# Kernel optimization log

Measured on AMD Instinct MI355X. Metric: run time of the kernel, lower is better.

## Reference

```python
import jax, jax.numpy as jnp
import numpy as np

HID = 512
HEADS = 8
PF = 2048
EPS = 1e-5


def _layernorm(x, g, b):
    mu = jnp.mean(x, axis=-1, keepdims=True)
    var = jnp.var(x, axis=-1, keepdims=True)
    return (x - mu) * jax.lax.rsqrt(var + EPS) * g + b


def setup_inputs() -> dict:
    key = jax.random.key(0)
    ks = jax.random.split(key, 20)
    s = 0.02
    inp = {
        "trg": jax.random.normal(ks[0], (16, 1024, HID), jnp.float32),
        "src": jax.random.normal(ks[1], (16, 1024, HID), jnp.float32),
        "ln_g": jnp.ones((HID,), jnp.float32),
        "ln_b": jnp.zeros((HID,), jnp.float32),
        "wq": jax.random.normal(ks[2], (HID, HID), jnp.float32) * s,
        "bq": jnp.zeros((HID,), jnp.float32),
        "wk": jax.random.normal(ks[3], (HID, HID), jnp.float32) * s,
        "bk": jnp.zeros((HID,), jnp.float32),
        "wv": jax.random.normal(ks[4], (HID, HID), jnp.float32) * s,
        "bv": jnp.zeros((HID,), jnp.float32),
        "wo": jax.random.normal(ks[5], (HID, HID), jnp.float32) * s,
        "bo": jnp.zeros((HID,), jnp.float32),
        "pf1_w": jax.random.normal(ks[6], (PF, HID), jnp.float32) * s,
        "pf1_b": jnp.zeros((PF,), jnp.float32),
        "pf2_w": jax.random.normal(ks[7], (HID, PF), jnp.float32) * s,
        "pf2_b": jnp.zeros((HID,), jnp.float32),
        "fc1_w": jax.random.normal(ks[8], (256, HID), jnp.float32) * s,
        "fc1_b": jnp.zeros((256,), jnp.float32),
        "fc2_w": jax.random.normal(ks[9], (2, 256), jnp.float32) * s,
        "fc2_b": jnp.zeros((2,), jnp.float32),
    }
    return inp


def reference(trg, src, ln_g, ln_b, wq, bq, wk, bk, wv, bv, wo, bo,
              pf1_w, pf1_b, pf2_w, pf2_b, fc1_w, fc1_b, fc2_w, fc2_b):
    B, T, D = trg.shape
    S = src.shape[1]
    dh = D // HEADS

    # --- multi-head attention (Q=trg, K=V=src, no mask; dropout=eval/no-op) ---
    q = (trg @ wq.T + bq).reshape(B, T, HEADS, dh)
    k = (src @ wk.T + bk).reshape(B, S, HEADS, dh)
    v = (src @ wv.T + bv).reshape(B, S, HEADS, dh)
    scores = jnp.einsum('bqhd,bkhd->bhqk', q, k) / jnp.sqrt(jnp.float32(dh))
    attn = jax.nn.softmax(scores, axis=-1)
    ctx = jnp.einsum('bhqk,bkhd->bqhd', attn, v).reshape(B, T, D)
    sa_out = ctx @ wo.T + bo

    x = _layernorm(trg + sa_out, ln_g, ln_b)

    # --- position-wise feed-forward ---
    h = jax.nn.relu(x @ pf1_w.T + pf1_b)
    ff = h @ pf2_w.T + pf2_b
    x = _layernorm(x + ff, ln_g, ln_b)

    # --- norm-weighted sum pooling over sequence (vectorized) ---
    norm = jnp.linalg.norm(x, axis=2)              # [B, T]
    w = jax.nn.softmax(norm, axis=1)               # [B, T]
    pooled = jnp.einsum('bt,btd->bd', w, x)        # [B, D]

    label = jax.nn.relu(pooled @ fc1_w.T + fc1_b) @ fc2_w.T + fc2_b
    return label
```

## Files before the change

kernel.cpp:

```cpp
#include <hip/hip_runtime.h>

typedef __bf16 bf16x8 __attribute__((ext_vector_type(8)));
typedef float f32x4 __attribute__((ext_vector_type(4)));
typedef unsigned short u16;

__device__ __forceinline__ u16 f2bf(float f){
  unsigned u = __builtin_bit_cast(unsigned, f);
  u += 0x7fffu + ((u>>16)&1u);
  return (u16)(u>>16);
}
__device__ __forceinline__ float bf2f(u16 h){
  unsigned u = ((unsigned)h)<<16; return __builtin_bit_cast(float,u);
}
__device__ __forceinline__ bf16x8 ld8(const u16* p){ return *(const bf16x8*)p; }
__device__ __forceinline__ f32x4 mfma16(bf16x8 a, bf16x8 b, f32x4 c){
  return __builtin_amdgcn_mfma_f32_16x16x32_bf16(a,b,c,0,0,0);
}
__device__ __forceinline__ void gl16(const u16* g, u16* l){
  __builtin_amdgcn_global_load_lds(
    (const __attribute__((address_space(1))) unsigned int*)g,
    (__attribute__((address_space(3))) unsigned int*)l, 16, 0, 0);
}
__device__ __forceinline__ unsigned cvtpk(float a, float b){
  unsigned r;
  asm("v_cvt_pk_bf16_f32 %0, %1, %2" : "=v"(r) : "v"(a), "v"(b));
  return r;
}

#define QSC 0.18033688f

template<int LO>
__global__ __launch_bounds__(256) void k_split(const float* __restrict__ x,
    u16* __restrict__ hi, u16* __restrict__ lo, int n){
  int i = (blockIdx.x*256 + threadIdx.x)*4;
  const int stride = gridDim.x*256*4;
  for(; i<n; i+=stride){
    float4 v = *(const float4*)(x+i);
    u16 h0=f2bf(v.x), h1=f2bf(v.y), h2=f2bf(v.z), h3=f2bf(v.w);
    ushort4 H = {h0,h1,h2,h3};
    *(ushort4*)(hi+i)=H;
    if constexpr(LO){
      ushort4 L = {f2bf(v.x-bf2f(h0)), f2bf(v.y-bf2f(h1)),
                   f2bf(v.z-bf2f(h2)), f2bf(v.w-bf2f(h3))};
      *(ushort4*)(lo+i)=L;
    }
  }
}

template<int EPI, int ALO, int BLO, int BK>
__global__ __launch_bounds__(256) void k_gemm(
  const u16* __restrict__ Ah, const u16* __restrict__ Al,
  const u16* __restrict__ Wh, const u16* __restrict__ Wl,
  const float* __restrict__ bias, int M, int N, int K,
  float* __restrict__ Cf, u16* __restrict__ Oh)
{
  constexpr int SL = BK/8;
  constexpr int SM = SL-1;
  constexpr int RPC = 512/BK;
  __shared__ __align__(16) u16 sAh[128*BK], sWh[128*BK];
  __shared__ __align__(16) u16 sAl[ALO?128*BK:8], sWl[BLO?128*BK:8];
  const int tid = threadIdx.x, w = tid>>6, l = tid&63;
  const int l15 = l&15, g = l>>4;
  const int gx = gridDim.x;
  const int bid = blockIdx.y*gx + blockIdx.x;
  const int nwg = gx*gridDim.y;
  const int wgid = (bid&7)*(nwg>>3) + (bid>>3);
  const int m0 = (wgid/gx)*128, n0 = (wgid%gx)*128;
  const int wr = (w>>1)*64, wc = (w&1)*64;
  f32x4 acc[4][4] = {};
  const int sr = l/SL, sslot = l&SM;
  const int scol = 8*(sslot ^ (sr&SM));
  for(int k0=0;k0<K;k0+=BK){
    #pragma unroll
    for(int i=0;i<BK/16;i++){
      const int rows = w*32 + i*RPC;
      const long ga = (long)(m0+rows+sr)*K + k0 + scol;
      const long gw = (long)(n0+rows+sr)*K + k0 + scol;
      gl16(Ah+ga, sAh + rows*BK);
      gl16(Wh+gw, sWh + rows*BK);
      if constexpr(ALO) gl16(Al+ga, sAl + rows*BK);
      if constexpr(BLO) gl16(Wl+gw, sWl + rows*BK);
    }
    __syncthreads();
    #pragma unroll
    for(int kk=0;kk<BK/32;kk++){
      const int ch8 = 8*((g+4*kk) ^ (l15&SM));
      bf16x8 ah[4], al[4];
      #pragma unroll
      for(int i=0;i<4;i++){
        const int o = (wr + i*16 + l15)*BK + ch8;
        ah[i] = *(const bf16x8*)(sAh + o);
        if constexpr(ALO) al[i] = *(const bf16x8*)(sAl + o);
      }
      #pragma unroll
      for(int j=0;j<4;j++){
        const int o = (wc + j*16 + l15)*BK + ch8;
        bf16x8 bh = *(const bf16x8*)(sWh + o);
        bf16x8 bl;
        if constexpr(BLO) bl = *(const bf16x8*)(sWl + o);
        #pragma unroll
        for(int i=0;i<4;i++){
          acc[i][j] = mfma16(ah[i], bh, acc[i][j]);
          if constexpr(ALO) acc[i][j] = mfma16(al[i], bh, acc[i][j]);
          if constexpr(BLO) acc[i][j] = mfma16(ah[i], bl, acc[i][j]);
        }
      }
    }
    __syncthreads();
  }
  #pragma unroll
  for(int i=0;i<4;i++){
    #pragma unroll
    for(int j=0;j<4;j++){
      const int col  = n0 + wc + j*16 + l15;
      const float bb = bias ? bias[col] : 0.f;
      const int rowb = m0 + wr + i*16 + g*4;
      #pragma unroll
      for(int jj=0;jj<4;jj++){
        float v = acc[i][j][jj] + bb;
        const int row = rowb + jj;
        if constexpr(EPI==0){ Cf[(long)row*N + col] = v; }
        else if constexpr(EPI==1){ Oh[(long)row*N + col] = f2bf(v); }
        else { Oh[(long)row*N + col] = f2bf(fmaxf(v,0.f)); }
      }
    }
  }
}

__global__ __launch_bounds__(256) void k_qkv(
  const u16* __restrict__ trg_hi, const u16* __restrict__ src_hi,
  const u16* __restrict__ Wh,
  const float* __restrict__ bq, const float* __restrict__ bk, const float* __restrict__ bv,
  u16* __restrict__ Qb, u16* __restrict__ Kb, u16* __restrict__ Vt)
{
  __shared__ __align__(16) u16 sAh[128*64], sWh[128*64];
  const int tid = threadIdx.x, w = tid>>6, l = tid&63;
  const int l15 = l&15, g = l>>4;
  const int bid = blockIdx.x;
  const int wgid = (bid&7)*192 + (bid>>3);
  const int m0 = (wgid/12)*128, n0 = (wgid%12)*128;
  const u16* Ah = (n0<512)? trg_hi : src_hi;
  const float* bp = (n0<512)? bq : (n0<1024? bk : bv);
  const int nb = (n0<512)? 0 : (n0<1024? 512 : 1024);
  const int wr = (w>>1)*64, wc = (w&1)*64;
  f32x4 acc[4][4] = {};
  const int sr = l>>3, sslot = l&7;
  const int scol = 8*(sslot ^ (sr&7));
  for(int k0=0;k0<512;k0+=64){
    #pragma unroll
    for(int i=0;i<4;i++){
      const int rows = w*32 + i*8;
      const long ga = (long)(m0+rows+sr)*512 + k0 + scol;
      const long gw = (long)(n0+rows+sr)*512 + k0 + scol;
      gl16(Ah+ga, sAh + rows*64);
      gl16(Wh+gw, sWh + rows*64);
    }
    __syncthreads();
    #pragma unroll
    for(int kk=0;kk<2;kk++){
      const int ch8 = 8*((g+4*kk) ^ (l15&7));
      bf16x8 ah[4];
      #pragma unroll
      for(int i=0;i<4;i++) ah[i] = *(const bf16x8*)(sAh + (wr + i*16 + l15)*64 + ch8);
      #pragma unroll
      for(int j=0;j<4;j++){
        bf16x8 bh = *(const bf16x8*)(sWh + (wc + j*16 + l15)*64 + ch8);
        #pragma unroll
        for(int i=0;i<4;i++){
          acc[i][j] = mfma16(ah[i], bh, acc[i][j]);
        }
      }
    }
    __syncthreads();
  }
  #pragma unroll
  for(int i=0;i<4;i++){
    #pragma unroll
    for(int j=0;j<4;j++){
      const int col = n0 + wc + j*16 + l15;
      const int cl  = col - nb;
      const float bb = bp[cl];
      const int rowb = m0 + wr + i*16 + g*4;
      #pragma unroll
      for(int jj=0;jj<4;jj++){
        float v = acc[i][j][jj] + bb;
        const int row = rowb + jj;
        if(n0 < 512){ Qb[(long)row*512 + cl] = f2bf(v*QSC); }
        else if(n0 < 1024){ Kb[(long)row*512 + cl] = f2bf(v); }
        else {
          const int h = cl>>6, d = cl&63;
          const long dst = (((long)(row>>10)*8 + h)*64 + d)*1024
                         + ((row>>6)&15)*64 + (row&15)*4 + ((row>>4)&3);
          Vt[dst] = f2bf(v);
        }
      }
    }
  }
}

__global__ __launch_bounds__(256) void k_attn(
  const u16* __restrict__ Q, const u16* __restrict__ K,
  const u16* __restrict__ Vt, u16* __restrict__ O)
{
  __shared__ __align__(16) u16 sK[64*64], sV[64*64];
  __shared__ __align__(16) u16 Ph[4][32*72];
  const int bid = blockIdx.x;
  const int wg = (bid&7)*128 + (bid>>3);
  const int q0 = (wg&7)*128, hd = (wg>>3)&7, b = wg>>6;
  const int tid = threadIdx.x, w = tid>>6, l = tid&63, l15 = l&15, g = l>>4;
  bf16x8 qf[2][2];
  #pragma unroll
  for(int rf=0;rf<2;rf++){
    const int qrow = q0 + rf*64 + w*16 + l15;
    const long qoff = (long)(b*1024 + qrow)*512 + hd*64 + g*8;
    qf[rf][0] = ld8(Q+qoff); qf[rf][1] = ld8(Q+qoff+32);
  }
  const int sr = l>>3, sslot = l&7;
  const int scol = 8*(sslot ^ (sr&7));
  const u16* Kb = K + (long)b*1024*512 + hd*64;
  const u16* Vb = Vt + (long)(b*8+hd)*64*1024;
  f32x4 rs[2] = {};
  f32x4 ctx[2][4] = {};
  for(int s0=0;s0<1024;s0+=64){
    #pragma unroll
    for(int i=0;i<2;i++){
      const int rows = w*8 + i*32;
      gl16(Kb + (long)(s0+rows+sr)*512 + scol, sK + rows*64);
      gl16(Vb + (long)(rows+sr)*1024 + s0 + scol, sV + rows*64);
    }
    __syncthreads();
    #pragma unroll
    for(int rf=0;rf<2;rf++){
      f32x4 sv[4];
      #pragma unroll
      for(int sf=0;sf<4;sf++){
        const int row = sf*16 + l15;
        f32x4 a = {};
        #pragma unroll
        for(int h=0;h<2;h++){
          const int ch = (g + 4*h) ^ (row&7);
          a = mfma16(qf[rf][h], *(const bf16x8*)(sK + row*64 + ch*8), a);
        }
        sv[sf] = a;
      }
      float p[4][4];
      #pragma unroll
      for(int sf=0;sf<4;sf++){
        #pragma unroll
        for(int j=0;j<4;j++){
          p[sf][j] = exp2f(sv[sf][j]);
          rs[rf][j] += p[sf][j];
        }
      }
      #pragma unroll
      for(int j=0;j<4;j++){
        uint2 pk = { cvtpk(p[0][j], p[1][j]), cvtpk(p[2][j], p[3][j]) };
        *(uint2*)(&Ph[w][(rf*16 + g*4 + j)*72 + l15*4]) = pk;
      }
    }
    #pragma unroll
    for(int ss=0;ss<2;ss++){
      bf16x8 pa0 = *(const bf16x8*)(&Ph[w][(     l15)*72 + ss*32 + g*8]);
      bf16x8 pa1 = *(const bf16x8*)(&Ph[w][(16 + l15)*72 + ss*32 + g*8]);
      #pragma unroll
      for(int df=0;df<4;df++){
        const int row = df*16 + l15;
        const int ch = (ss*4 + g) ^ (row&7);
        const bf16x8 vf = *(const bf16x8*)(sV + row*64 + ch*8);
        ctx[0][df] = mfma16(pa0, vf, ctx[0][df]);
        ctx[1][df] = mfma16(pa1, vf, ctx[1][df]);
      }
    }
    __syncthreads();
  }
  #pragma unroll
  for(int rf=0;rf<2;rf++){
    float inv[4];
    #pragma unroll
    for(int j=0;j<4;j++){
      float t = rs[rf][j];
      #pragma unroll
      for(int mask=1;mask<16;mask<<=1) t += __shfl_xor(t, mask);
      inv[j] = 1.f/t;
    }
    #pragma unroll
    for(int df=0;df<4;df++){
      #pragma unroll
      for(int j=0;j<4;j++){
        const float v = ctx[rf][df][j] * inv[j];
        const long off = (long)(b*1024 + q0 + rf*64 + w*16 + g*4 + j)*512 + hd*64 + df*16 + l15;
        O[off] = f2bf(v);
      }
    }
  }
}

__global__ __launch_bounds__(256) void k_ln(
  const float* __restrict__ xa, const float* __restrict__ xb,
  const float* __restrict__ gg, const float* __restrict__ bvec,
  float* __restrict__ yf, u16* __restrict__ yh,
  float* __restrict__ norms)
{
  const int w = threadIdx.x>>6, l = threadIdx.x&63;
  const long rrow = (long)blockIdx.x*4 + w;
  const long base = rrow*512 + l*8;
  float4 a0 = *(const float4*)(xa+base), a1 = *(const float4*)(xa+base+4);
  float4 b0 = *(const float4*)(xb+base), b1 = *(const float4*)(xb+base+4);
  float v[8] = {a0.x+b0.x, a0.y+b0.y, a0.z+b0.z, a0.w+b0.w,
                a1.x+b1.x, a1.y+b1.y, a1.z+b1.z, a1.w+b1.w};
  float s=0.f, q=0.f;
  #pragma unroll
  for(int j=0;j<8;j++){ s += v[j]; q += v[j]*v[j]; }
  #pragma unroll
  for(int mask=1;mask<64;mask<<=1){ s += __shfl_xor(s,mask); q += __shfl_xor(q,mask); }
  const float mu  = s*(1.f/512.f);
  const float var = q*(1.f/512.f) - mu*mu;
  const float rstd = rsqrtf(var + 1e-5f);
  float y[8]; float nq = 0.f;
  #pragma unroll
  for(int j=0;j<8;j++){
    const int c = l*8+j;
    y[j] = (v[j]-mu)*rstd*gg[c] + bvec[c];
    nq += y[j]*y[j];
  }
  float4 t0={y[0],y[1],y[2],y[3]}, t1={y[4],y[5],y[6],y[7]};
  *(float4*)(yf+base)=t0; *(float4*)(yf+base+4)=t1;
  if(yh){
    u16 hv[8];
    #pragma unroll
    for(int j=0;j<8;j++){ hv[j]=f2bf(y[j]); }
    ushort4 hh0={hv[0],hv[1],hv[2],hv[3]}, hh1={hv[4],hv[5],hv[6],hv[7]};
    *(ushort4*)(yh+base)=hh0; *(ushort4*)(yh+base+4)=hh1;
  }
  if(norms){
    #pragma unroll
    for(int mask=1;mask<64;mask<<=1) nq += __shfl_xor(nq,mask);
    if(l==0) norms[rrow] = sqrtf(nq);
  }
}

__global__ __launch_bounds__(256) void k_pool(const float* __restrict__ x2,
   const float* __restrict__ norms, float* __restrict__ pooled)
{
  const int b = blockIdx.y;
  const int col = blockIdx.x*256 + threadIdx.x;
  __shared__ float wsm[1024];
  __shared__ float red[4];
  const int tid = threadIdx.x, w = tid>>6, l = tid&63;
  float lm = -1e30f;
  for(int i=tid;i<1024;i+=256){ const float n = norms[b*1024+i]; wsm[i]=n; lm=fmaxf(lm,n); }
  #pragma unroll
  for(int mask=1;mask<64;mask<<=1) lm = fmaxf(lm, __shfl_xor(lm,mask));
  __syncthreads();
  if(l==0) red[w]=lm;
  __syncthreads();
  const float bm = fmaxf(fmaxf(red[0],red[1]), fmaxf(red[2],red[3]));
  __syncthreads();
  float ls = 0.f;
  for(int i=tid;i<1024;i+=256){ const float e = __expf(wsm[i]-bm); wsm[i]=e; ls+=e; }
  #pragma unroll
  for(int mask=1;mask<64;mask<<=1) ls += __shfl_xor(ls,mask);
  __syncthreads();
  if(l==0) red[w]=ls;
  __syncthreads();
  const float inv = 1.f/(red[0]+red[1]+red[2]+red[3]);
  float acc = 0.f;
  for(int t=0;t<1024;t++) acc += wsm[t]*x2[((long)b*1024+t)*512 + col];
  pooled[b*512+col] = acc*inv;
}

__global__ __launch_bounds__(256) void k_head(const float* __restrict__ pooled,
  const float* __restrict__ w1, const float* __restrict__ b1,
  const float* __restrict__ w2, const float* __restrict__ b2,
  float* __restrict__ out)
{
  __shared__ float ps[16*512];
  __shared__ float h1[16*256];
  const int tid = threadIdx.x;
  for(int i=tid;i<16*512;i+=256) ps[i]=pooled[i];
  __syncthreads();
  float acc[16] = {};
  for(int k=0;k<512;k++){
    const float wv = w1[tid*512+k];
    #pragma unroll
    for(int i=0;i<16;i++) acc[i] += ps[i*512+k]*wv;
  }
  #pragma unroll
  for(int i=0;i<16;i++) h1[i*256+tid] = fmaxf(acc[i]+b1[tid], 0.f);
  __syncthreads();
  if(tid<32){
    const int i = tid>>1, o = tid&1;
    float a = b2[o];
    for(int k=0;k<256;k++) a += h1[i*256+k]*w2[o*256+k];
    out[i*2+o] = a;
  }
}

extern "C" void kernel_launch(void* const* d_in, const int* in_sizes, int n_in,
                              void* d_out, int out_size, void* d_ws, size_t ws_size,
                              hipStream_t stream)
{
  const float* trg  = (const float*)d_in[0];
  const float* src  = (const float*)d_in[1];
  const float* ln_g = (const float*)d_in[2];
  const float* ln_b = (const float*)d_in[3];
  const float* wq   = (const float*)d_in[4];  const float* bq  = (const float*)d_in[5];
  const float* wk   = (const float*)d_in[6];  const float* bk  = (const float*)d_in[7];
  const float* wv   = (const float*)d_in[8];  const float* bv  = (const float*)d_in[9];
  const float* wo   = (const float*)d_in[10]; const float* bo  = (const float*)d_in[11];
  const float* pf1w = (const float*)d_in[12]; const float* pf1b= (const float*)d_in[13];
  const float* pf2w = (const float*)d_in[14]; const float* pf2b= (const float*)d_in[15];
  const float* fc1w = (const float*)d_in[16]; const float* fc1b= (const float*)d_in[17];
  const float* fc2w = (const float*)d_in[18]; const float* fc2b= (const float*)d_in[19];
  float* out = (float*)d_out;

  char* ws = (char*)d_ws;
  const size_t PL = (size_t)16384*512*2;
  auto P = [&](int i)->u16*{ return (u16*)(ws + (size_t)i*PL); };
  u16 *src_hi=P(0), *trg_hi=P(1);
  u16 *Qb=P(2), *Kb=P(3), *Vt=P(4), *ctx=P(5);
  float* sa  = (float*)(ws + 0*PL);
  float* x1f = (float*)(ws + 2*PL);
  u16 *x1_hi = P(4);
  u16 *h_hi  = P(5);
  float* ffb = (float*)(ws + 0*PL);
  float* x2  = (float*)(ws + 5*PL);
  size_t off = 9*PL;
  auto carve = [&](size_t n)->char*{ char* p = ws+off; off += n; return p; };
  u16* wqkv_hi=(u16*)carve((size_t)1536*512*2);
  u16* wo_hi=(u16*)carve(512*512*2);
  u16* p1_hi=(u16*)carve((size_t)2048*512*2);
  u16* p2_hi=(u16*)carve((size_t)512*2048*2);
  float* norms  = (float*)carve(16384*4);
  float* pooled = (float*)carve(16*512*4);
  (void)ws_size; (void)in_sizes; (void)n_in; (void)out_size;

  const int NTOK = 16384;

  k_split<0><<<dim3(8192),256,0,stream>>>(trg, trg_hi, nullptr, NTOK*512);
  k_split<0><<<dim3(8192),256,0,stream>>>(src, src_hi, nullptr, NTOK*512);
  k_split<0><<<dim3(256),256,0,stream>>>(wq, wqkv_hi,          nullptr, 512*512);
  k_split<0><<<dim3(256),256,0,stream>>>(wk, wqkv_hi+512*512,  nullptr, 512*512);
  k_split<0><<<dim3(256),256,0,stream>>>(wv, wqkv_hi+1024*512, nullptr, 512*512);
  k_split<0><<<dim3(256),256,0,stream>>>(wo, wo_hi, nullptr, 512*512);
  k_split<0><<<dim3(1024),256,0,stream>>>(pf1w, p1_hi, nullptr, 2048*512);
  k_split<0><<<dim3(1024),256,0,stream>>>(pf2w, p2_hi, nullptr, 512*2048);

  k_qkv<<<dim3(1536),256,0,stream>>>(trg_hi,src_hi,wqkv_hi,bq,bk,bv,Qb,Kb,Vt);

  k_attn<<<dim3(1024),256,0,stream>>>(Qb,Kb,Vt,ctx);

  k_gemm<0,0,0,64><<<dim3(4,128),256,0,stream>>>(ctx,nullptr,wo_hi,nullptr,bo,NTOK,512,512,sa,nullptr);
  k_ln<<<dim3(4096),256,0,stream>>>(trg, sa, ln_g, ln_b, x1f, x1_hi, nullptr);

  k_gemm<2,0,0,64><<<dim3(16,128),256,0,stream>>>(x1_hi,nullptr,p1_hi,nullptr,pf1b,NTOK,2048,512,nullptr,h_hi);
  k_gemm<0,0,0,64><<<dim3(4,128),256,0,stream>>>(h_hi,nullptr,p2_hi,nullptr,pf2b,NTOK,512,2048,ffb,nullptr);
  k_ln<<<dim3(4096),256,0,stream>>>(x1f, ffb, ln_g, ln_b, x2, nullptr, norms);

  k_pool<<<dim3(2,16),256,0,stream>>>(x2, norms, pooled);
  k_head<<<1,256,0,stream>>>(pooled, fc1w, fc1b, fc2w, fc2b, out);
}
```

Baseline: 375.0 us.

## Double-buffer K/V tiles in attention and split pooling over sequence chunks

The attention kernel now keeps two LDS buffers for K and V. It prefetches the next 64-key tile with async global-to-LDS loads while the current tile is computed, which drops the barrier that sat between each load and its compute. The pooling kernel, which ran only 32 blocks that each walked 1024 rows serially, is split into 8 sequence chunks that write partial sums. A small new kernel then adds those partials. This trades more LDS use (which may lower attention occupancy), an extra launch and a partial buffer for more parallelism and overlap.

```diff
diff --git a/kernel.cpp b/kernel.cpp
--- a/kernel.cpp
+++ b/kernel.cpp
@@ -202,7 +202,7 @@
   const u16* __restrict__ Q, const u16* __restrict__ K,
   const u16* __restrict__ Vt, u16* __restrict__ O)
 {
-  __shared__ __align__(16) u16 sK[64*64], sV[64*64];
+  __shared__ __align__(16) u16 sK[2][64*64], sV[2][64*64];
   __shared__ __align__(16) u16 Ph[4][32*72];
   const int bid = blockIdx.x;
   const int wg = (bid&7)*128 + (bid>>3);
@@ -221,14 +221,24 @@
   const u16* Vb = Vt + (long)(b*8+hd)*64*1024;
   f32x4 rs[2] = {};
   f32x4 ctx[2][4] = {};
-  for(int s0=0;s0<1024;s0+=64){
-    #pragma unroll
-    for(int i=0;i<2;i++){
-      const int rows = w*8 + i*32;
-      gl16(Kb + (long)(s0+rows+sr)*512 + scol, sK + rows*64);
-      gl16(Vb + (long)(rows+sr)*1024 + s0 + scol, sV + rows*64);
-    }
-    __syncthreads();
+  #pragma unroll
+  for(int i=0;i<2;i++){
+    const int rows = w*8 + i*32;
+    gl16(Kb + (long)(rows+sr)*512 + scol, sK[0] + rows*64);
+    gl16(Vb + (long)(rows+sr)*1024 + scol, sV[0] + rows*64);
+  }
+  __syncthreads();
+  for(int t=0;t<16;t++){
+    const int cur = t&1;
+    if(t<15){
+      const int s1 = (t+1)*64;
+      #pragma unroll
+      for(int i=0;i<2;i++){
+        const int rows = w*8 + i*32;
+        gl16(Kb + (long)(s1+rows+sr)*512 + scol, sK[cur^1] + rows*64);
+        gl16(Vb + (long)(rows+sr)*1024 + s1 + scol, sV[cur^1] + rows*64);
+      }
+    }
     #pragma unroll
     for(int rf=0;rf<2;rf++){
       f32x4 sv[4];
@@ -239,7 +249,7 @@
         #pragma unroll
         for(int h=0;h<2;h++){
           const int ch = (g + 4*h) ^ (row&7);
-          a = mfma16(qf[rf][h], *(const bf16x8*)(sK + row*64 + ch*8), a);
+          a = mfma16(qf[rf][h], *(const bf16x8*)(sK[cur] + row*64 + ch*8), a);
         }
         sv[sf] = a;
       }
@@ -266,7 +276,7 @@
       for(int df=0;df<4;df++){
         const int row = df*16 + l15;
         const int ch = (ss*4 + g) ^ (row&7);
-        const bf16x8 vf = *(const bf16x8*)(sV + row*64 + ch*8);
+        const bf16x8 vf = *(const bf16x8*)(sV[cur] + row*64 + ch*8);
         ctx[0][df] = mfma16(pa0, vf, ctx[0][df]);
         ctx[1][df] = mfma16(pa1, vf, ctx[1][df]);
       }
@@ -339,10 +349,10 @@
   }
 }
 
-__global__ __launch_bounds__(256) void k_pool(const float* __restrict__ x2,
-   const float* __restrict__ norms, float* __restrict__ pooled)
-{
-  const int b = blockIdx.y;
+__global__ __launch_bounds__(256) void k_pool2(const float* __restrict__ x2,
+   const float* __restrict__ norms, float* __restrict__ partial)
+{
+  const int b = blockIdx.y, tc = blockIdx.z;
   const int col = blockIdx.x*256 + threadIdx.x;
   __shared__ float wsm[1024];
   __shared__ float red[4];
@@ -365,8 +375,19 @@
   __syncthreads();
   const float inv = 1.f/(red[0]+red[1]+red[2]+red[3]);
   float acc = 0.f;
-  for(int t=0;t<1024;t++) acc += wsm[t]*x2[((long)b*1024+t)*512 + col];
-  pooled[b*512+col] = acc*inv;
+  const int t0 = tc*128;
+  for(int t=t0;t<t0+128;t++) acc += wsm[t]*x2[((long)b*1024+t)*512 + col];
+  partial[((long)tc*16 + b)*512 + col] = acc*inv;
+}
+
+__global__ __launch_bounds__(256) void k_poolr(const float* __restrict__ partial,
+   float* __restrict__ pooled)
+{
+  const int i = blockIdx.x*256 + threadIdx.x;
+  float a = 0.f;
+  #pragma unroll
+  for(int tc=0;tc<8;tc++) a += partial[tc*8192 + i];
+  pooled[i] = a;
 }
 
 __global__ __launch_bounds__(256) void k_head(const float* __restrict__ pooled,
@@ -432,6 +453,7 @@
   u16* p1_hi=(u16*)carve((size_t)2048*512*2);
   u16* p2_hi=(u16*)carve((size_t)512*2048*2);
   float* norms  = (float*)carve(16384*4);
+  float* partial= (float*)carve(8*16*512*4);
   float* pooled = (float*)carve(16*512*4);
   (void)ws_size; (void)in_sizes; (void)n_in; (void)out_size;
 
@@ -457,6 +479,7 @@
   k_gemm<0,0,0,64><<<dim3(4,128),256,0,stream>>>(h_hi,nullptr,p2_hi,nullptr,pf2b,NTOK,512,2048,ffb,nullptr);
   k_ln<<<dim3(4096),256,0,stream>>>(x1f, ffb, ln_g, ln_b, x2, nullptr, norms);
 
-  k_pool<<<dim3(2,16),256,0,stream>>>(x2, norms, pooled);
+  k_pool2<<<dim3(2,16,8),256,0,stream>>>(x2, norms, partial);
+  k_poolr<<<dim3(32),256,0,stream>>>(partial, pooled);
   k_head<<<1,256,0,stream>>>(pooled, fc1w, fc1b, fc2w, fc2b, out);
 }
```

Result: faster. 354.3 us (-5.5%).
